# Kernel optimization log

Measured on AMD Instinct MI355X. Metric: run time of the kernel, lower is better.

The kernel has to match this reference:

```python
import jax, jax.numpy as jnp
import numpy as np
from jax import lax

B, S, H, SS, DS = 512, 200, 128, 2, 2  # batch, seq_len, hidden, static_size, dynamic_size

def _xavier(k, shape):
    fan_in, fan_out = shape[-1], shape[0]
    lim = float(np.sqrt(6.0 / (fan_in + fan_out)))
    return jax.random.uniform(k, shape, jnp.float32, -lim, lim)

def setup_inputs() -> dict:
    key = jax.random.key(0)
    ks = jax.random.split(key, 20)
    return {
        "static":  jax.random.uniform(ks[0], (B, SS, S), jnp.float32),
        "dynamic": jax.random.uniform(ks[1], (B, DS, S), jnp.float32),
        # Encoder: 1x1 Conv1d weights stored as [H, C] (kernel dim squeezed)
        "sW": _xavier(ks[2], (H, SS)),  "sb": jnp.zeros((H,), jnp.float32),
        "dW": _xavier(ks[3], (H, DS)),  "db": jnp.zeros((H,), jnp.float32),
        # Decoder learned initial output / hidden
        "x0": _xavier(ks[4], (1, SS)),  "h0": _xavier(ks[5], (1, H)),
        # Decoder input embedding Linear(SS -> H)
        "Wemb": _xavier(ks[6], (H, SS)), "bemb": jnp.zeros((H,), jnp.float32),
        # GRU (1 layer): torch layout [3H, H] gates ordered (r, z, n)
        "Wih": _xavier(ks[7], (3 * H, H)), "Whh": _xavier(ks[8], (3 * H, H)),
        "bih": jnp.zeros((3 * H,), jnp.float32), "bhh": jnp.zeros((3 * H,), jnp.float32),
        # Attention: v [H], W [H, 3H]
        "Wa": _xavier(ks[9], (H, 3 * H)), "va": _xavier(ks[10], (1, H))[0],
        # Decoder pointer head: v [H], W [H, 2H]
        "Wd": _xavier(ks[11], (H, 2 * H)), "vd": _xavier(ks[12], (1, H))[0],
    }

def _decode(static, dynamic, sW, sb, dW, db, x0, h0, Wemb, bemb,
            Wih, Whh, bih, bhh, Wa, va, Wd, vd):
    # Encoder: 1x1 convs == per-node linear maps  -> [B, H, S]
    static_enc  = jnp.einsum('hc,bcs->bhs', sW, static)  + sb[None, :, None]
    dynamic_enc = jnp.einsum('hc,bcs->bhs', dW, dynamic) + db[None, :, None]

    keys = jax.random.split(jax.random.key(42), S)  # one sample key per decode step
    static_sg = lax.stop_gradient(static)           # mirrors static.data gather in torch

    def step(carry, key):
        last_out, h = carry                              # [B,SS], [B,H]
        emb = last_out @ Wemb.T + bemb                   # [B,H]
        # GRU cell (torch gate order r, z, n)
        gi = emb @ Wih.T + bih                           # [B,3H]
        gh = h @ Whh.T + bhh
        r = jax.nn.sigmoid(gi[:, :H] + gh[:, :H])
        z = jax.nn.sigmoid(gi[:, H:2 * H] + gh[:, H:2 * H])
        n = jnp.tanh(gi[:, 2 * H:] + r * gh[:, 2 * H:])
        h_new = (1.0 - z) * n + z * h                    # [B,H]
        # Additive attention over nodes (vectorized over batch)
        hid = jnp.broadcast_to(h_new[:, :, None], (B, H, S))
        energy = jnp.concatenate([static_enc, dynamic_enc, hid], axis=1)   # [B,3H,S]
        attn = jax.nn.softmax(
            jnp.einsum('h,bhs->bs', va, jnp.tanh(jnp.einsum('hk,bks->bhs', Wa, energy))),
            axis=1)                                      # [B,S]
        context = jnp.einsum('bs,bhs->bh', attn, static_enc)               # [B,H]
        ctx = jnp.concatenate(
            [static_enc, jnp.broadcast_to(context[:, :, None], (B, H, S))], axis=1)  # [B,2H,S]
        logits = jnp.einsum('h,bhs->bs', vd,
                            jnp.tanh(jnp.einsum('hk,bks->bhs', Wd, ctx)))  # [B,S]
        # mask is all ones (mask_fn=None) -> log(mask)=0
        probs = jax.nn.softmax(logits, axis=1)
        idx = jax.random.categorical(key, logits, axis=1)                  # [B] int
        next_out = jnp.take_along_axis(static_sg, idx[:, None, None], axis=2)[:, :, 0]  # [B,SS]
        chosen_p = jnp.take_along_axis(probs, idx[:, None], axis=1)[:, 0]  # [B]
        return (next_out, h_new), (idx, chosen_p)

    init = (jnp.broadcast_to(x0, (B, SS)), jnp.broadcast_to(h0, (B, H)))
    _, (idx_seq, prob_seq) = lax.scan(step, init, keys)
    return idx_seq.T, prob_seq.T                          # [B,S] each

def reference(static, dynamic, sW, sb, dW, db, x0, h0, Wemb, bemb,
              Wih, Whh, bih, bhh, Wa, va, Wd, vd):
    return _decode(static, dynamic, sW, sb, dW, db, x0, h0, Wemb, bemb,
                   Wih, Whh, bih, bhh, Wa, va, Wd, vd)
```

## Files before the change

kernel.cpp:

```cpp
#include <hip/hip_runtime.h>
#include <stdint.h>
#include <math.h>

#define NB 512
#define NS 200
#define NH 128
#define NH3 384
#define NWAVE 8
#define PF 8

#define IDX4(h) ((h) + (((h) >> 6) << 2))
#define IDX1(h) ((h) + (((h) >> 6) << 4))

__device__ __forceinline__ float xla_tanhf(float x) {
  float cx = fminf(fmaxf(x, -9.0f), 9.0f);
  float x2 = __fmul_rn(cx, cx);
  float p = -2.76076847742355e-16f;
  p = __fadd_rn(__fmul_rn(x2, p), 2.00018790482477e-13f);
  p = __fadd_rn(__fmul_rn(x2, p), -8.60467152213735e-11f);
  p = __fadd_rn(__fmul_rn(x2, p), 5.12229709037114e-08f);
  p = __fadd_rn(__fmul_rn(x2, p), 1.48572235717979e-05f);
  p = __fadd_rn(__fmul_rn(x2, p), 6.37261928875436e-04f);
  p = __fadd_rn(__fmul_rn(x2, p), 4.89352455891786e-03f);
  p = __fmul_rn(cx, p);
  float q = 1.19825839466702e-06f;
  q = __fadd_rn(__fmul_rn(x2, q), 1.18534705686654e-04f);
  q = __fadd_rn(__fmul_rn(x2, q), 2.26843463243900e-03f);
  q = __fadd_rn(__fmul_rn(x2, q), 4.89352518554385e-03f);
  float r = __fdiv_rn(p, q);
  return (fabsf(x) < 0.0004f) ? x : r;
}

__device__ __forceinline__ float xla_sigmoidf(float x) {
  return __fadd_rn(0.5f, __fmul_rn(0.5f, xla_tanhf(__fmul_rn(0.5f, x))));
}

__device__ __forceinline__ float fast_tanhf(float x) {
  float cx = fminf(fmaxf(x, -9.0f), 9.0f);
  float x2 = __fmul_rn(cx, cx);
  float p = fmaf(x2, -2.76076847742355e-16f, 2.00018790482477e-13f);
  p = fmaf(x2, p, -8.60467152213735e-11f);
  p = fmaf(x2, p, 5.12229709037114e-08f);
  p = fmaf(x2, p, 1.48572235717979e-05f);
  p = fmaf(x2, p, 6.37261928875436e-04f);
  p = fmaf(x2, p, 4.89352455891786e-03f);
  p = __fmul_rn(cx, p);
  float q = fmaf(x2, 1.19825839466702e-06f, 1.18534705686654e-04f);
  q = fmaf(x2, q, 2.26843463243900e-03f);
  q = fmaf(x2, q, 4.89352518554385e-03f);
  float r = __builtin_amdgcn_rcpf(q);
  float e = fmaf(-q, r, 1.0f);
  r = fmaf(r, e, r);
  return __fmul_rn(p, r);
}

__device__ __forceinline__ uint32_t rotl32(uint32_t v, int r) {
  return (v << r) | (v >> (32 - r));
}
__device__ __forceinline__ void threefry2x32(uint32_t k0, uint32_t k1,
                                             uint32_t x0, uint32_t x1,
                                             uint32_t& o0, uint32_t& o1) {
  uint32_t k2 = k0 ^ k1 ^ 0x1BD11BDAu;
  x0 += k0; x1 += k1;
  #define TFR(r) { x0 += x1; x1 = rotl32(x1, r); x1 ^= x0; }
  TFR(13) TFR(15) TFR(26) TFR(6)
  x0 += k1; x1 += k2 + 1u;
  TFR(17) TFR(29) TFR(16) TFR(24)
  x0 += k2; x1 += k0 + 2u;
  TFR(13) TFR(15) TFR(26) TFR(6)
  x0 += k0; x1 += k1 + 3u;
  TFR(17) TFR(29) TFR(16) TFR(24)
  x0 += k1; x1 += k2 + 4u;
  TFR(13) TFR(15) TFR(26) TFR(6)
  x0 += k2; x1 += k0 + 5u;
  #undef TFR
  o0 = x0; o1 = x1;
}

__device__ __forceinline__ float bits_to_gumbel(uint32_t bits) {
  const float kTiny = 1.1754943508222875e-38f;
  float f = __fsub_rn(__uint_as_float((bits >> 9) | 0x3F800000u), 1.0f);
  float u = __fadd_rn(__fmul_rn(f, __fsub_rn(1.0f, kTiny)), kTiny);
  u = fmaxf(kTiny, u);
  return -logf(-logf(u));
}

__global__ __launch_bounds__(512, 4) void k_decode(
    const float* __restrict__ stat, const float* __restrict__ dyn,
    const float* __restrict__ sW,   const float* __restrict__ sb,
    const float* __restrict__ dW,   const float* __restrict__ db,
    const float* __restrict__ x0,   const float* __restrict__ h0,
    const float* __restrict__ Wemb, const float* __restrict__ bemb,
    const float* __restrict__ Wih,  const float* __restrict__ Whh,
    const float* __restrict__ bih,  const float* __restrict__ bhh,
    const float* __restrict__ Wa,   const float* __restrict__ va,
    const float* __restrict__ Wd,   const float* __restrict__ vd,
    float* __restrict__ out) {

  __shared__ __align__(16) float st0L[NS], st1L[NS], dy0L[NS], dy1L[NS];
  __shared__ float4 AF4p[132];
  __shared__ float4 DF4p[132];
  __shared__ float4 CW4[NH];
  __shared__ float  vaP[144];
  __shared__ float  AcL[NH];
  __shared__ float WembL[2*NH], bembL[NH];
  __shared__ float bihL[NH3], bhhL[NH3];
  __shared__ __align__(16) float embL[NH], hL[NH];
  __shared__ float giL[NH3], ghL[NH3];
  __shared__ float HtLp[144];
  __shared__ float ex2L[NS];
  __shared__ uint32_t keysL[2*NS];
  __shared__ float xpL[2];
  __shared__ float part[NWAVE][8];
  __shared__ int   partI[NWAVE];

  const int t = threadIdx.x;
  const int b = blockIdx.x;
  const int w = t >> 6;
  const int s = t >> 1;
  const int h0i = (t & 1) * 64;
  const int b4 = h0i + ((h0i >> 6) << 2);
  const int b1 = h0i + ((h0i >> 6) << 4);
  const bool activeS = (t < 2*NS);

  if (t < NS) {
    st0L[t] = stat[(size_t)b*2*NS + t];
    st1L[t] = stat[(size_t)b*2*NS + NS + t];
    dy0L[t] = dyn[(size_t)b*2*NS + t];
    dy1L[t] = dyn[(size_t)b*2*NS + NS + t];
    uint32_t q0, q1;
    threefry2x32(0u, 42u, 0u, (uint32_t)t, q0, q1);
    keysL[2*t] = q0; keysL[2*t + 1] = q1;
  }
  if (t < NH) {
    int h = t;
    const float* war = Wa + (size_t)h * NH3;
    float as0 = 0.f, as1 = 0.f, ad0 = 0.f, ad1 = 0.f, ac = 0.f;
    for (int k = 0; k < NH; ++k) {
      as0 = fmaf(war[k],     sW[k*2+0], as0);
      as1 = fmaf(war[k],     sW[k*2+1], as1);
      ad0 = fmaf(war[NH+k],  dW[k*2+0], ad0);
      ad1 = fmaf(war[NH+k],  dW[k*2+1], ad1);
      ac  = fmaf(war[k],     sb[k],     ac);
    }
    for (int k = 0; k < NH; ++k) ac = fmaf(war[NH+k], db[k], ac);
    AF4p[IDX4(h)] = make_float4(as0, as1, ad0, ad1);
    vaP[IDX1(h)] = va[h];
    AcL[h] = ac;

    const float* wdr = Wd + (size_t)h * 256;
    float ds0 = 0.f, ds1 = 0.f, dc = 0.f, c0 = 0.f, c1 = 0.f, cb = 0.f;
    for (int k = 0; k < NH; ++k) {
      ds0 = fmaf(wdr[k],    sW[k*2+0], ds0);
      ds1 = fmaf(wdr[k],    sW[k*2+1], ds1);
      dc  = fmaf(wdr[k],    sb[k],     dc);
      c0  = fmaf(wdr[NH+k], sW[k*2+0], c0);
      c1  = fmaf(wdr[NH+k], sW[k*2+1], c1);
      cb  = fmaf(wdr[NH+k], sb[k],     cb);
    }
    DF4p[IDX4(h)] = make_float4(ds0, ds1, vd[h], dc);
    CW4[h] = make_float4(c0, c1, cb, 0.f);

    bembL[h] = bemb[h];
    WembL[2*h]   = Wemb[2*h];
    WembL[2*h+1] = Wemb[2*h+1];
    hL[h] = h0[h];
  }
  for (int i = t; i < NH3; i += 512) { bihL[i] = bih[i]; bhhL[i] = bhh[i]; }
  if (t == 0) { xpL[0] = x0[0]; xpL[1] = x0[1]; }
  __syncthreads();

  float s0r = 0.f, s1r = 0.f, d0r = 0.f, d1r = 0.f;
  if (activeS) { s0r = st0L[s]; s1r = st1L[s]; d0r = dy0L[s]; d1r = dy1L[s]; }

  float4 wreg[PF];
  {
    const float4* wpA = (t < NH3) ? (const float4*)(Wih + (size_t)t * NH)
                                  : (const float4*)(Whh + (size_t)(t - NH3) * NH);
    #pragma unroll
    for (int i = 0; i < PF; ++i) wreg[i] = wpA[i];
  }

  for (int step = 0; step < NS; ++step) {
    if (t < NH) {
      float e = fmaf(xpL[1], WembL[t*2+1], __fmul_rn(xpL[0], WembL[t*2+0]));
      embL[t] = __fadd_rn(e, bembL[t]);
    }
    __syncthreads();

    if (t < 256) {
      const float4* wp0 = (const float4*)(Wih + (size_t)t * NH);
      const float4* wp1 = (const float4*)(Whh + (size_t)(NH + t) * NH);
      const float4* e4 = (const float4*)embL;
      const float4* h4 = (const float4*)hL;
      float a0 = 0.f, a1 = 0.f;
      #pragma unroll
      for (int k4 = 0; k4 < PF; ++k4) {
        float4 c0 = wreg[k4], c1 = wp1[k4];
        float4 ev = e4[k4],   hv = h4[k4];
        a0 = fmaf(c0.x, ev.x, a0); a0 = fmaf(c0.y, ev.y, a0);
        a0 = fmaf(c0.z, ev.z, a0); a0 = fmaf(c0.w, ev.w, a0);
        a1 = fmaf(c1.x, hv.x, a1); a1 = fmaf(c1.y, hv.y, a1);
        a1 = fmaf(c1.z, hv.z, a1); a1 = fmaf(c1.w, hv.w, a1);
      }
      #pragma unroll 8
      for (int k4 = PF; k4 < 32; ++k4) {
        float4 c0 = wp0[k4], c1 = wp1[k4];
        float4 ev = e4[k4],  hv = h4[k4];
        a0 = fmaf(c0.x, ev.x, a0); a0 = fmaf(c0.y, ev.y, a0);
        a0 = fmaf(c0.z, ev.z, a0); a0 = fmaf(c0.w, ev.w, a0);
        a1 = fmaf(c1.x, hv.x, a1); a1 = fmaf(c1.y, hv.y, a1);
        a1 = fmaf(c1.z, hv.z, a1); a1 = fmaf(c1.w, hv.w, a1);
      }
      giL[t]      = __fadd_rn(a0, bihL[t]);
      ghL[NH + t] = __fadd_rn(a1, bhhL[NH + t]);
    } else {
      const bool isWih = (t < NH3);
      const float4* wp = isWih
          ? (const float4*)(Wih + (size_t)t * NH)
          : (const float4*)(Whh + (size_t)(t - NH3) * NH);
      const float4* op = isWih ? (const float4*)embL : (const float4*)hL;
      float a0 = 0.f;
      #pragma unroll
      for (int k4 = 0; k4 < PF; ++k4) {
        float4 c = wreg[k4], v = op[k4];
        a0 = fmaf(c.x, v.x, a0); a0 = fmaf(c.y, v.y, a0);
        a0 = fmaf(c.z, v.z, a0); a0 = fmaf(c.w, v.w, a0);
      }
      #pragma unroll 8
      for (int k4 = PF; k4 < 32; ++k4) {
        float4 c = wp[k4], v = op[k4];
        a0 = fmaf(c.x, v.x, a0); a0 = fmaf(c.y, v.y, a0);
        a0 = fmaf(c.z, v.z, a0); a0 = fmaf(c.w, v.w, a0);
      }
      if (isWih) giL[t]       = __fadd_rn(a0, bihL[t]);
      else       ghL[t - NH3] = __fadd_rn(a0, bhhL[t - NH3]);
    }
    __syncthreads();

    if (t < NH) {
      float r = xla_sigmoidf(__fadd_rn(giL[t],      ghL[t]));
      float z = xla_sigmoidf(__fadd_rn(giL[t+NH],   ghL[t+NH]));
      float n = xla_tanhf(__fadd_rn(giL[t+2*NH], __fmul_rn(r, ghL[t+2*NH])));
      float hv = hL[t];
      hL[t] = __fadd_rn(__fmul_rn(__fsub_rn(1.0f, z), n), __fmul_rn(z, hv));
    }
    __syncthreads();

    if (t < NH) {
      const float4* war = (const float4*)(Wa + (size_t)t*NH3 + 2*NH);
      const float4* hn4 = (const float4*)hL;
      float acc = 0.f;
      #pragma unroll 8
      for (int k4 = 0; k4 < 32; ++k4) {
        float4 a = war[k4], hv = hn4[k4];
        acc = fmaf(a.x, hv.x, acc); acc = fmaf(a.y, hv.y, acc);
        acc = fmaf(a.z, hv.z, acc); acc = fmaf(a.w, hv.w, acc);
      }
      HtLp[IDX1(t)] = __fadd_rn(acc, AcL[t]);
    }
    __syncthreads();

    float acc = 0.f;
    if (activeS) {
      #pragma unroll 4
      for (int j = 0; j < 64; ++j) {
        float4 af = AF4p[b4 + j];
        float vah = vaP[b1 + j];
        float ath = HtLp[b1 + j];
        float e = fmaf(af.y, s1r, __fmul_rn(af.x, s0r));
        e = fmaf(af.z, d0r, e);
        e = fmaf(af.w, d1r, e);
        e = __fadd_rn(e, ath);
        acc = fmaf(vah, fast_tanhf(e), acc);
      }
    }
    float sc = activeS ? __fadd_rn(acc, __shfl_xor(acc, 1)) : 0.f;

    float exv = activeS ? expf(sc) : 0.f;
    {
      float sm = exv;
      float c0 = __fmul_rn(exv, s0r);
      float c1 = __fmul_rn(exv, s1r);
      #pragma unroll
      for (int mm = 2; mm < 64; mm <<= 1) {
        sm = __fadd_rn(sm, __shfl_xor(sm, mm));
        c0 = __fadd_rn(c0, __shfl_xor(c0, mm));
        c1 = __fadd_rn(c1, __shfl_xor(c1, mm));
      }
      if ((t & 63) == 0) { part[w][0] = sm; part[w][1] = c0; part[w][2] = c1; }
    }
    __syncthreads();

    if (t < NH) {
      float sume = part[0][0], r0 = part[0][1], r1 = part[0][2];
      #pragma unroll
      for (int ww = 1; ww < NWAVE; ++ww) {
        sume = __fadd_rn(sume, part[ww][0]);
        r0   = __fadd_rn(r0,   part[ww][1]);
        r1   = __fadd_rn(r1,   part[ww][2]);
      }
      r0 = __fdiv_rn(r0, sume); r1 = __fdiv_rn(r1, sume);
      float4 cw = CW4[t];
      float ct = fmaf(r0, cw.x, fmaf(r1, cw.y, cw.z));
      HtLp[IDX1(t)] = __fadd_rn(DF4p[IDX4(t)].w, ct);
    }
    __syncthreads();

    float accD = 0.f;
    if (activeS) {
      #pragma unroll 4
      for (int j = 0; j < 64; ++j) {
        float4 df = DF4p[b4 + j];
        float ctd = HtLp[b1 + j];
        float d = fmaf(df.y, s1r, __fmul_rn(df.x, s0r));
        d = __fadd_rn(d, ctd);
        accD = fmaf(df.z, fast_tanhf(d), accD);
      }
    }
    float sc2 = activeS ? __fadd_rn(accD, __shfl_xor(accD, 1)) : 0.f;

    float e2 = activeS ? expf(sc2) : 0.f;
    if (activeS && (t & 1) == 0) ex2L[s] = e2;
    {
      uint32_t k0 = keysL[2*step], k1 = keysL[2*step + 1];
      float gv = -INFINITY;
      int gidx = 1 << 20;
      if (activeS) {
        uint32_t q0, q1;
        threefry2x32(k0, k1, 0u, (uint32_t)(b*NS + s), q0, q1);
        gv = __fadd_rn(bits_to_gumbel(q0 ^ q1), sc2);
        gidx = s;
      }
      float sm = e2;
      #pragma unroll
      for (int mm = 2; mm < 64; mm <<= 1) {
        sm = __fadd_rn(sm, __shfl_xor(sm, mm));
        float ov = __shfl_xor(gv, mm); int oi = __shfl_xor(gidx, mm);
        if (ov > gv || (ov == gv && oi < gidx)) { gv = ov; gidx = oi; }
      }
      if ((t & 63) == 0) { part[w][3] = sm; part[w][4] = gv; partI[w] = gidx; }
    }
    __syncthreads();

    if (t == 0) {
      float bv = part[0][4]; int bi = partI[0];
      float sume2 = part[0][3];
      #pragma unroll
      for (int ww = 1; ww < NWAVE; ++ww) {
        float vv = part[ww][4]; int ii = partI[ww];
        if (vv > bv || (vv == bv && ii < bi)) { bv = vv; bi = ii; }
        sume2 = __fadd_rn(sume2, part[ww][3]);
      }
      out[(size_t)b*NS + step] = (float)bi;
      out[(size_t)NB*NS + (size_t)b*NS + step] = __fdiv_rn(ex2L[bi], sume2);
      xpL[0] = st0L[bi]; xpL[1] = st1L[bi];
    }
    __syncthreads();
  }
}

extern "C" void kernel_launch(void* const* d_in, const int* in_sizes, int n_in,
                              void* d_out, int out_size, void* d_ws, size_t ws_size,
                              hipStream_t stream) {
  (void)in_sizes; (void)n_in; (void)out_size; (void)d_ws; (void)ws_size;
  const float* stat = (const float*)d_in[0];
  const float* dyn  = (const float*)d_in[1];
  const float* sW   = (const float*)d_in[2];
  const float* sb   = (const float*)d_in[3];
  const float* dW   = (const float*)d_in[4];
  const float* db   = (const float*)d_in[5];
  const float* x0   = (const float*)d_in[6];
  const float* h0   = (const float*)d_in[7];
  const float* Wemb = (const float*)d_in[8];
  const float* bemb = (const float*)d_in[9];
  const float* Wih  = (const float*)d_in[10];
  const float* Whh  = (const float*)d_in[11];
  const float* bih  = (const float*)d_in[12];
  const float* bhh  = (const float*)d_in[13];
  const float* Wa   = (const float*)d_in[14];
  const float* va   = (const float*)d_in[15];
  const float* Wd   = (const float*)d_in[16];
  const float* vd   = (const float*)d_in[17];
  float* out = (float*)d_out;

  k_decode<<<NB, 512, 0, stream>>>(stat, dyn, sW, sb, dW, db, x0, h0,
                                   Wemb, bemb, Wih, Whh, bih, bhh,
                                   Wa, va, Wd, vd, out);
}
```

Baseline: 6.715 ms.

## Use exp-based fast tanh, fast __expf, and drop register-cached GRU weights

Replaces the rational-polynomial fast_tanhf in the attention and pointer loops with a formula built from __expf and a hardware reciprocal. Switches the softmax exponentials to __expf. Removes the per-thread register prefetch of the first GRU weight chunk, so every step reads all weights from global memory. The aim is to shorten the hot tanh loops, at some accuracy risk for the sampled indices. Dropping the register cache may add memory traffic but frees registers.

```diff
diff --git a/kernel.cpp b/kernel.cpp
--- a/kernel.cpp
+++ b/kernel.cpp
@@ -7,7 +7,6 @@
 #define NH 128
 #define NH3 384
 #define NWAVE 8
-#define PF 8
 
 #define IDX4(h) ((h) + (((h) >> 6) << 2))
 #define IDX1(h) ((h) + (((h) >> 6) << 4))
@@ -36,22 +35,9 @@
 }
 
 __device__ __forceinline__ float fast_tanhf(float x) {
-  float cx = fminf(fmaxf(x, -9.0f), 9.0f);
-  float x2 = __fmul_rn(cx, cx);
-  float p = fmaf(x2, -2.76076847742355e-16f, 2.00018790482477e-13f);
-  p = fmaf(x2, p, -8.60467152213735e-11f);
-  p = fmaf(x2, p, 5.12229709037114e-08f);
-  p = fmaf(x2, p, 1.48572235717979e-05f);
-  p = fmaf(x2, p, 6.37261928875436e-04f);
-  p = fmaf(x2, p, 4.89352455891786e-03f);
-  p = __fmul_rn(cx, p);
-  float q = fmaf(x2, 1.19825839466702e-06f, 1.18534705686654e-04f);
-  q = fmaf(x2, q, 2.26843463243900e-03f);
-  q = fmaf(x2, q, 4.89352518554385e-03f);
-  float r = __builtin_amdgcn_rcpf(q);
-  float e = fmaf(-q, r, 1.0f);
-  r = fmaf(r, e, r);
-  return __fmul_rn(p, r);
+  float e = __expf(__fmul_rn(x, 2.0f));
+  float r = __builtin_amdgcn_rcpf(__fadd_rn(e, 1.0f));
+  return fmaf(-2.0f, r, 1.0f);
 }
 
 __device__ __forceinline__ uint32_t rotl32(uint32_t v, int r) {
@@ -173,14 +159,6 @@
   float s0r = 0.f, s1r = 0.f, d0r = 0.f, d1r = 0.f;
   if (activeS) { s0r = st0L[s]; s1r = st1L[s]; d0r = dy0L[s]; d1r = dy1L[s]; }
 
-  float4 wreg[PF];
-  {
-    const float4* wpA = (t < NH3) ? (const float4*)(Wih + (size_t)t * NH)
-                                  : (const float4*)(Whh + (size_t)(t - NH3) * NH);
-    #pragma unroll
-    for (int i = 0; i < PF; ++i) wreg[i] = wpA[i];
-  }
-
   for (int step = 0; step < NS; ++step) {
     if (t < NH) {
       float e = fmaf(xpL[1], WembL[t*2+1], __fmul_rn(xpL[0], WembL[t*2+0]));
@@ -194,17 +172,8 @@
       const float4* e4 = (const float4*)embL;
       const float4* h4 = (const float4*)hL;
       float a0 = 0.f, a1 = 0.f;
-      #pragma unroll
-      for (int k4 = 0; k4 < PF; ++k4) {
-        float4 c0 = wreg[k4], c1 = wp1[k4];
-        float4 ev = e4[k4],   hv = h4[k4];
-        a0 = fmaf(c0.x, ev.x, a0); a0 = fmaf(c0.y, ev.y, a0);
-        a0 = fmaf(c0.z, ev.z, a0); a0 = fmaf(c0.w, ev.w, a0);
-        a1 = fmaf(c1.x, hv.x, a1); a1 = fmaf(c1.y, hv.y, a1);
-        a1 = fmaf(c1.z, hv.z, a1); a1 = fmaf(c1.w, hv.w, a1);
-      }
       #pragma unroll 8
-      for (int k4 = PF; k4 < 32; ++k4) {
+      for (int k4 = 0; k4 < 32; ++k4) {
         float4 c0 = wp0[k4], c1 = wp1[k4];
         float4 ev = e4[k4],  hv = h4[k4];
         a0 = fmaf(c0.x, ev.x, a0); a0 = fmaf(c0.y, ev.y, a0);
@@ -221,14 +190,8 @@
           : (const float4*)(Whh + (size_t)(t - NH3) * NH);
       const float4* op = isWih ? (const float4*)embL : (const float4*)hL;
       float a0 = 0.f;
-      #pragma unroll
-      for (int k4 = 0; k4 < PF; ++k4) {
-        float4 c = wreg[k4], v = op[k4];
-        a0 = fmaf(c.x, v.x, a0); a0 = fmaf(c.y, v.y, a0);
-        a0 = fmaf(c.z, v.z, a0); a0 = fmaf(c.w, v.w, a0);
-      }
       #pragma unroll 8
-      for (int k4 = PF; k4 < 32; ++k4) {
+      for (int k4 = 0; k4 < 32; ++k4) {
         float4 c = wp[k4], v = op[k4];
         a0 = fmaf(c.x, v.x, a0); a0 = fmaf(c.y, v.y, a0);
         a0 = fmaf(c.z, v.z, a0); a0 = fmaf(c.w, v.w, a0);
@@ -277,7 +240,7 @@
     }
     float sc = activeS ? __fadd_rn(acc, __shfl_xor(acc, 1)) : 0.f;
 
-    float exv = activeS ? expf(sc) : 0.f;
+    float exv = activeS ? __expf(sc) : 0.f;
     {
       float sm = exv;
       float c0 = __fmul_rn(exv, s0r);
@@ -320,7 +283,7 @@
     }
     float sc2 = activeS ? __fadd_rn(accD, __shfl_xor(accD, 1)) : 0.f;
 
-    float e2 = activeS ? expf(sc2) : 0.f;
+    float e2 = activeS ? __expf(sc2) : 0.f;
     if (activeS && (t & 1) == 0) ex2L[s] = e2;
     {
       uint32_t k0 = keysL[2*step], k1 = keysL[2*step + 1];
```

After: 6.057 ms. -9.8%, faster.
